# Optimization experiments

Hardware: AMD Instinct MI355X
Metric: run time of the kernel (lower is better)

The kernel has to match this reference:

```python
import jax, jax.numpy as jnp
import numpy as np


def setup_inputs() -> dict:
    key = jax.random.key(0)
    k1, k2, k3, k4, k5, k6 = jax.random.split(key, 6)
    B, S, I, H = 64, 512, 1024, 1024
    scale_ih = 1.0 / np.sqrt(I)
    scale_hh = 1.0 / np.sqrt(H)
    return {
        "inputs": jax.random.normal(k1, (B, S, I), dtype=jnp.float32),
        "h0": jax.random.normal(k2, (1, B, H), dtype=jnp.float32),
        "weight_ih": jax.random.normal(k3, (H, I), dtype=jnp.float32) * scale_ih,
        "weight_hh": jax.random.normal(k4, (H, H), dtype=jnp.float32) * scale_hh,
        "bias_ih": jax.random.normal(k5, (H,), dtype=jnp.float32) * 0.01,
        "bias_hh": jax.random.normal(k6, (H,), dtype=jnp.float32) * 0.01,
    }


def reference(inputs, h0, weight_ih, weight_hh, bias_ih, bias_hh):
    # Elman RNN with ReLU: h_t = relu(x_t W_ih^T + b_ih + h_{t-1} W_hh^T + b_hh)
    # inputs: [B, S, I]; h0: [1, B, H]
    # Precompute the input projection for all timesteps in one big GEMM.
    x_proj = jnp.einsum('bsi,hi->bsh', inputs, weight_ih) + bias_ih + bias_hh  # [B,S,H]

    def step(h, xp_t):
        h_new = jax.nn.relu(xp_t + jnp.matmul(h, weight_hh.T))  # [B,H]
        return h_new, h_new

    h_init = h0[0]  # [B, H]
    h_last, outs = jax.lax.scan(step, h_init, jnp.swapaxes(x_proj, 0, 1))  # outs: [S,B,H]
    outputs = jnp.swapaxes(outs, 0, 1)  # [B, S, H]
    h_n = h_last[None]  # [1, B, H]
    return outputs, h_n
```

## Files before the change

### kernel.cpp

```cpp
#include <hip/hip_runtime.h>
#include <hip/hip_bf16.h>
#include <stdint.h>

#define BATCH 64
#define SEQ   512
#define INDIM 1024
#define HDIM  1024
#define NBLK  256
#define NGRP  8
#define GSLOT 32
#define FPAD  16
#define GBUF_U16 32768
#define GBUF_DW  16384

typedef short bf16x8 __attribute__((ext_vector_type(8)));
typedef short s16x4  __attribute__((ext_vector_type(4)));
typedef float f32x4  __attribute__((ext_vector_type(4)));
typedef unsigned short u16;
typedef unsigned int   u32;
typedef u32 u32x4 __attribute__((ext_vector_type(4)));
typedef u16 u16x4 __attribute__((ext_vector_type(4)));

static __device__ __forceinline__ u16 f2bf(float x) {
  unsigned int u = __float_as_uint(x);
  u += 0x7fffu + ((u >> 16) & 1u);
  return (u16)(u >> 16);
}
static __device__ __forceinline__ float bf2f(u16 b) {
  return __uint_as_float(((unsigned int)b) << 16);
}

static __device__ __forceinline__ int coh_ld_i32(const int* p) {
  int v;
  asm volatile("global_load_dword %0, %1, off sc0 sc1\n\t"
               "s_waitcnt vmcnt(0)"
               : "=&v"(v) : "v"(p) : "memory");
  return v;
}

static __device__ __forceinline__ void split4(float4 v, u16x4& hi, u16x4& lo) {
  hi.x = f2bf(v.x); lo.x = f2bf(v.x - bf2f(hi.x));
  hi.y = f2bf(v.y); lo.y = f2bf(v.y - bf2f(hi.y));
  hi.z = f2bf(v.z); lo.z = f2bf(v.z - bf2f(hi.z));
  hi.w = f2bf(v.w); lo.w = f2bf(v.w - bf2f(hi.w));
}
static __device__ __forceinline__ bf16x8 ld8(const u16* p) {
  s16x4 a = *(const s16x4*)p;
  s16x4 b = *(const s16x4*)(p + 4);
  return __builtin_shufflevector(a, b, 0, 1, 2, 3, 4, 5, 6, 7);
}

__global__ void init0(int* __restrict__ flags, int n) {
  int i = blockIdx.x * blockDim.x + threadIdx.x;
  if (i < n) flags[i] = 0;
}

__global__ void init1(const float* __restrict__ h0, u32* __restrict__ hw) {
  int i = blockIdx.x * blockDim.x + threadIdx.x;
  if (i < BATCH * HDIM) {
    int b = i >> 10, k = i & 1023;
    int g = b >> 3, r = b & 7;
    int k32 = k >> 5, kg = (k >> 3) & 3, j = k & 7;
    float x = h0[i];
    u16 hi = f2bf(x);
    u16 lo = f2bf(x - bf2f(hi));
    size_t di = (size_t)g * (2 * GBUF_DW) + (size_t)((k32 * 64 + kg * 16 + r) * 8 + j);
    hw[di] = (u32)hi | ((u32)lo << 16);
  }
}

__global__ __launch_bounds__(256) void xproj_kernel(const float* __restrict__ A,
                                                    const float* __restrict__ W,
                                                    const float* __restrict__ bih,
                                                    const float* __restrict__ bhh,
                                                    float* __restrict__ C) {
  __shared__ u16 Ah[4][128][12], Al[4][128][12], Bh[4][128][12], Bl[4][128][12];
  const int nb = blockIdx.x;
  const int mb = blockIdx.y;
  const int m_base = mb * 128, n_base = nb * 128;
  const int tid = (int)threadIdx.x;
  const int wid = tid >> 6, lane = tid & 63;
  const int wm = wid >> 1, wn = wid & 1;
  const int r = lane & 15, kg = lane >> 4;
  const int srow = tid >> 1;
  const int skq  = (tid & 1) * 16;

  const float* ap0 = A + (size_t)(m_base + srow) * INDIM + skq;
  const float* bp0 = W + (size_t)(n_base + srow) * INDIM + skq;

  f32x4 acc[4][4] = {};

  for (int k0 = 0; k0 < INDIM; k0 += 32) {
    float4 av[4], bv[4];
#pragma unroll
    for (int i = 0; i < 4; ++i) {
      av[i] = *(const float4*)(ap0 + k0 + i * 4);
      bv[i] = *(const float4*)(bp0 + k0 + i * 4);
    }
    __syncthreads();
#pragma unroll
    for (int i = 0; i < 4; ++i) {
      int kk = skq + i * 4;
      int kgw = kk >> 3, off = kk & 7;
      u16x4 hi, lo;
      split4(av[i], hi, lo);
      *(u16x4*)&Ah[kgw][srow][off] = hi;
      *(u16x4*)&Al[kgw][srow][off] = lo;
      split4(bv[i], hi, lo);
      *(u16x4*)&Bh[kgw][srow][off] = hi;
      *(u16x4*)&Bl[kgw][srow][off] = lo;
    }
    __syncthreads();

    bf16x8 ah[4], al[4], bhv[4], blv[4];
#pragma unroll
    for (int mf = 0; mf < 4; ++mf) {
      int row = wm * 64 + mf * 16 + r;
      ah[mf] = ld8(&Ah[kg][row][0]);
      al[mf] = ld8(&Al[kg][row][0]);
    }
#pragma unroll
    for (int nf = 0; nf < 4; ++nf) {
      int row = wn * 64 + nf * 16 + r;
      bhv[nf] = ld8(&Bh[kg][row][0]);
      blv[nf] = ld8(&Bl[kg][row][0]);
    }
#pragma unroll
    for (int mf = 0; mf < 4; ++mf)
#pragma unroll
      for (int nf = 0; nf < 4; ++nf) {
        acc[mf][nf] = __builtin_amdgcn_mfma_f32_16x16x32_bf16(ah[mf], bhv[nf], acc[mf][nf], 0, 0, 0);
        acc[mf][nf] = __builtin_amdgcn_mfma_f32_16x16x32_bf16(ah[mf], blv[nf], acc[mf][nf], 0, 0, 0);
        acc[mf][nf] = __builtin_amdgcn_mfma_f32_16x16x32_bf16(al[mf], bhv[nf], acc[mf][nf], 0, 0, 0);
      }
  }

#pragma unroll
  for (int nf = 0; nf < 4; ++nf) {
    int col = n_base + wn * 64 + nf * 16 + r;
    float bias = bih[col] + bhh[col];
#pragma unroll
    for (int mf = 0; mf < 4; ++mf) {
      int rowb = m_base + wm * 64 + mf * 16 + kg * 4;
#pragma unroll
      for (int q = 0; q < 4; ++q) {
        C[(size_t)(rowb + q) * HDIM + col] = acc[mf][nf][q] + bias;
      }
    }
  }
}

__global__ __launch_bounds__(512, 1) void rnn_scan(
    const float* __restrict__ Whh, float* __restrict__ out,
    u16* hbase, int* flags) {
  __shared__ u16 WH[32][2][64][8], WL[32][2][64][8];
  __shared__ __align__(16) float red[2][8][2][8][20];

  const int blk = (int)blockIdx.x;
  const int grp = blk & 7;
  const int slot = blk >> 3;
  const int n0 = slot * 32;
  const int tid = (int)threadIdx.x;
  const int wv = tid >> 6, lane = tid & 63;
  const int r = lane & 15, kg = lane >> 4;
  const bool zrow = r >= 8;

  for (int it = 0; it < 16; ++it) {
    int f4 = it * 512 + tid;
    int row = f4 >> 8;
    int k0 = (f4 & 255) * 4;
    float4 v = *(const float4*)(Whh + (size_t)(n0 + row) * HDIM + k0);
    int k32 = k0 >> 5, kgg = (k0 >> 3) & 3, j = k0 & 7;
    int nt = row >> 4, ln = kgg * 16 + (row & 15);
    u16x4 hi, lo;
    split4(v, hi, lo);
    *(u16x4*)&WH[k32][nt][ln][j] = hi;
    *(u16x4*)&WL[k32][nt][ln][j] = lo;
  }
  __syncthreads();

  u16* const hb0 = hbase + (size_t)grp * (2 * GBUF_U16);
  u16* const hb1 = hb0 + GBUF_U16;
  int* const gflag = flags + grp * (GSLOT * 4) * FPAD;
  const int* const pollp = gflag + ((wv << 4) + (lane & 15)) * FPAD;

  const int eid = wv * 64 + lane;
  const int er = (eid >> 5) & 7;
  const int ec = eid & 31;
  const float* xpbase = out + ((size_t)(grp * 8 + er) * SEQ) * HDIM + n0 + ec;
  float xfCur = 0.f, xfNext = 0.f, sPrev = 0.f;
  if (wv < 4) xfCur = xpbase[0];

  for (int t = 0; t < SEQ; ++t) {
    const int p2 = t & 1;
    const u16* hc = (t & 1) ? hb1 : hb0;
    u16* hn = (t & 1) ? hb0 : hb1;

    if (t > 0) {
      int v;
      do { v = coh_ld_i32(pollp); } while (!__all(v >= t));
    }

    u32x4 P0, P1, P2, P3, P4, P5, P6, P7;
    if (!zrow) {
      const char* a0 = (const char*)hc + (size_t)((wv * 4) * 64 + lane) * 32;
      const char* a1 = a0 + 4096;
      asm volatile(
          "global_load_dwordx4 %0, %8, off sc0 sc1\n\t"
          "global_load_dwordx4 %1, %8, off offset:16 sc0 sc1\n\t"
          "global_load_dwordx4 %2, %8, off offset:2048 sc0 sc1\n\t"
          "global_load_dwordx4 %3, %8, off offset:2064 sc0 sc1\n\t"
          "global_load_dwordx4 %4, %9, off sc0 sc1\n\t"
          "global_load_dwordx4 %5, %9, off offset:16 sc0 sc1\n\t"
          "global_load_dwordx4 %6, %9, off offset:2048 sc0 sc1\n\t"
          "global_load_dwordx4 %7, %9, off offset:2064 sc0 sc1"
          : "=&v"(P0), "=&v"(P1), "=&v"(P2), "=&v"(P3),
            "=&v"(P4), "=&v"(P5), "=&v"(P6), "=&v"(P7)
          : "v"(a0), "v"(a1)
          : "memory");
      asm volatile("s_waitcnt vmcnt(0)"
          : "+v"(P0), "+v"(P1), "+v"(P2), "+v"(P3),
            "+v"(P4), "+v"(P5), "+v"(P6), "+v"(P7));
    } else {
      P0 = P1 = P2 = P3 = P4 = P5 = P6 = P7 = (u32x4){0, 0, 0, 0};
    }

    if (wv < 4) {
      if (t > 0)
        __builtin_nontemporal_store(sPrev, (float*)(xpbase + (size_t)(t - 1) * HDIM));
      if (t + 1 < SEQ) xfNext = xpbase[(size_t)(t + 1) * HDIM];
    }

    f32x4 acc0 = {0.f, 0.f, 0.f, 0.f};
    f32x4 acc1 = {0.f, 0.f, 0.f, 0.f};
#define DO_K32(i, QA, QB)                                                      \
    {                                                                          \
      u32 d0 = QA[0], d1 = QA[1], d2 = QA[2], d3 = QA[3];                      \
      u32 d4 = QB[0], d5 = QB[1], d6 = QB[2], d7 = QB[3];                      \
      union { u32 w[4]; bf16x8 v; } AH, AL;                                    \
      AH.w[0] = (d0 & 0xFFFFu) | (d1 << 16);                                   \
      AH.w[1] = (d2 & 0xFFFFu) | (d3 << 16);                                   \
      AH.w[2] = (d4 & 0xFFFFu) | (d5 << 16);                                   \
      AH.w[3] = (d6 & 0xFFFFu) | (d7 << 16);                                   \
      AL.w[0] = (d0 >> 16) | (d1 & 0xFFFF0000u);                               \
      AL.w[1] = (d2 >> 16) | (d3 & 0xFFFF0000u);                               \
      AL.w[2] = (d4 >> 16) | (d5 & 0xFFFF0000u);                               \
      AL.w[3] = (d6 >> 16) | (d7 & 0xFFFF0000u);                               \
      int k32 = wv * 4 + (i);                                                  \
      bf16x8 b0h = *(const bf16x8*)&WH[k32][0][lane][0];                       \
      bf16x8 b0l = *(const bf16x8*)&WL[k32][0][lane][0];                       \
      bf16x8 b1h = *(const bf16x8*)&WH[k32][1][lane][0];                       \
      bf16x8 b1l = *(const bf16x8*)&WL[k32][1][lane][0];                       \
      acc0 = __builtin_amdgcn_mfma_f32_16x16x32_bf16(AH.v, b0h, acc0, 0, 0, 0);\
      acc0 = __builtin_amdgcn_mfma_f32_16x16x32_bf16(AH.v, b0l, acc0, 0, 0, 0);\
      acc0 = __builtin_amdgcn_mfma_f32_16x16x32_bf16(AL.v, b0h, acc0, 0, 0, 0);\
      acc1 = __builtin_amdgcn_mfma_f32_16x16x32_bf16(AH.v, b1h, acc1, 0, 0, 0);\
      acc1 = __builtin_amdgcn_mfma_f32_16x16x32_bf16(AH.v, b1l, acc1, 0, 0, 0);\
      acc1 = __builtin_amdgcn_mfma_f32_16x16x32_bf16(AL.v, b1h, acc1, 0, 0, 0);\
    }
    DO_K32(0, P0, P1)
    DO_K32(1, P2, P3)
    DO_K32(2, P4, P5)
    DO_K32(3, P6, P7)
#undef DO_K32

    if (kg < 2) {
#pragma unroll
      for (int q = 0; q < 4; ++q) {
        red[p2][wv][0][kg * 4 + q][r] = acc0[q];
        red[p2][wv][1][kg * 4 + q][r] = acc1[q];
      }
    }
    __syncthreads();

    if (wv < 4) {
      float s = xfCur;
#pragma unroll
      for (int w = 0; w < 8; ++w) s += red[p2][w][ec >> 4][er][ec & 15];
      s = s > 0.f ? s : 0.f;
      sPrev = s;
      u16 hi = f2bf(s);
      u16 lo = f2bf(s - bf2f(hi));
      u32 dw = (u32)hi | ((u32)lo << 16);
      u32* hp = (u32*)hn + (size_t)((slot * 64 + (ec >> 3) * 16 + er) * 8 + (ec & 7));
      asm volatile("global_store_dword %0, %1, off sc1\n\t"
                   "s_waitcnt vmcnt(0)"
                   :: "v"(hp), "v"(dw) : "memory");
      if (lane == 0) {
        int* fp = gflag + (slot * 4 + wv) * FPAD;
        int tv = t + 1;
        asm volatile("global_store_dword %0, %1, off sc0 sc1"
                     :: "v"(fp), "v"(tv) : "memory");
      }
      xfCur = xfNext;
    }
  }

  if (wv < 4)
    __builtin_nontemporal_store(sPrev, (float*)(xpbase + (size_t)(SEQ - 1) * HDIM));
}

__global__ void copy_hn(const float* __restrict__ out, float* __restrict__ hn) {
  int idx = blockIdx.x * blockDim.x + threadIdx.x;
  if (idx < BATCH * HDIM) {
    int b = idx >> 10, j = idx & 1023;
    hn[idx] = out[((size_t)b * SEQ + (SEQ - 1)) * (size_t)HDIM + j];
  }
}

extern "C" void kernel_launch(void* const* d_in, const int* in_sizes, int n_in,
                              void* d_out, int out_size, void* d_ws, size_t ws_size,
                              hipStream_t stream) {
  const float* inputs = (const float*)d_in[0];
  const float* h0     = (const float*)d_in[1];
  const float* w_ih   = (const float*)d_in[2];
  const float* w_hh   = (const float*)d_in[3];
  const float* b_ih   = (const float*)d_in[4];
  const float* b_hh   = (const float*)d_in[5];

  float* outBase = (float*)d_out;
  float* hnBase  = outBase + (size_t)BATCH * SEQ * HDIM;

  u16* hbase = (u16*)d_ws;
  int* flags = (int*)(hbase + (size_t)NGRP * 2 * GBUF_U16);
  const int nflags = NGRP * GSLOT * 4 * FPAD;

  init0<<<(nflags + 255) / 256, 256, 0, stream>>>(flags, nflags);
  init1<<<(BATCH * HDIM + 255) / 256, 256, 0, stream>>>(h0, (u32*)hbase);

  xproj_kernel<<<dim3(8, 256), 256, 0, stream>>>(inputs, w_ih, b_ih, b_hh, outBase);

  const float* wha = w_hh;
  float* oa = outBase;
  u16* hba = hbase;
  int* fa = flags;
  void* args[4] = {&wha, &oa, &hba, &fa};
  (void)hipLaunchCooperativeKernel((const void*)rnn_scan, dim3(NBLK), dim3(512), args, 0, stream);

  copy_hn<<<256, 256, 0, stream>>>(outBase, hnBase);
}
```

Measured before the change: 1.917 ms.

## Warp-specialize RNN scan into compute, epilogue, and I/O waves with skewed pipeline

The scan kernel now splits its 8 waves by role. Waves 0-3 do the MFMA matvec over K=256 each, waves 4-5 reduce, apply ReLU, split to bf16 hi/lo and publish h with flags, and waves 6-7 prefetch x_proj and write outputs through shared buffers. The epilogue for step t-1 runs concurrently with the matvec for step t, one step behind, so global I/O and the reduction leave the critical path. The trade-off is half as many waves on the MFMA and longer per-wave load chains. The flag count per slot also drops, which changes the polling pattern.

```diff
diff --git a/kernel.cpp b/kernel.cpp
--- a/kernel.cpp
+++ b/kernel.cpp
@@ -10,14 +10,15 @@
 #define NGRP  8
 #define GSLOT 32
 #define FPAD  16
-#define GBUF_U16 32768
-#define GBUF_DW  16384
+#define SLAB_BYTES 32768
 
 typedef short bf16x8 __attribute__((ext_vector_type(8)));
 typedef short s16x4  __attribute__((ext_vector_type(4)));
+typedef float f32x2  __attribute__((ext_vector_type(2)));
 typedef float f32x4  __attribute__((ext_vector_type(4)));
 typedef unsigned short u16;
 typedef unsigned int   u32;
+typedef u32 u32x2 __attribute__((ext_vector_type(2)));
 typedef u32 u32x4 __attribute__((ext_vector_type(4)));
 typedef u16 u16x4 __attribute__((ext_vector_type(4)));
 
@@ -64,7 +65,7 @@
     float x = h0[i];
     u16 hi = f2bf(x);
     u16 lo = f2bf(x - bf2f(hi));
-    size_t di = (size_t)g * (2 * GBUF_DW) + (size_t)((k32 * 64 + kg * 16 + r) * 8 + j);
+    size_t di = (size_t)g * (SLAB_BYTES / 4) + (size_t)(k32 * 256 + kg * 64 + r * 8 + j);
     hw[di] = (u32)hi | ((u32)lo << 16);
   }
 }
@@ -152,9 +153,11 @@
 
 __global__ __launch_bounds__(512, 1) void rnn_scan(
     const float* __restrict__ Whh, float* __restrict__ out,
-    u16* hbase, int* flags) {
+    char* ring, int* flags) {
   __shared__ u16 WH[32][2][64][8], WL[32][2][64][8];
-  __shared__ __align__(16) float red[2][8][2][8][20];
+  __shared__ __align__(16) float red[2][4][2][8][20];
+  __shared__ __align__(8) float xfbuf[2][8][32];
+  __shared__ __align__(8) float sbuf[2][8][32];
 
   const int blk = (int)blockIdx.x;
   const int grp = blk & 7;
@@ -162,8 +165,6 @@
   const int n0 = slot * 32;
   const int tid = (int)threadIdx.x;
   const int wv = tid >> 6, lane = tid & 63;
-  const int r = lane & 15, kg = lane >> 4;
-  const bool zrow = r >= 8;
 
   for (int it = 0; it < 16; ++it) {
     int f4 = it * 512 + tid;
@@ -179,125 +180,156 @@
   }
   __syncthreads();
 
-  u16* const hb0 = hbase + (size_t)grp * (2 * GBUF_U16);
-  u16* const hb1 = hb0 + GBUF_U16;
-  int* const gflag = flags + grp * (GSLOT * 4) * FPAD;
-  const int* const pollp = gflag + ((wv << 4) + (lane & 15)) * FPAD;
-
-  const int eid = wv * 64 + lane;
-  const int er = (eid >> 5) & 7;
-  const int ec = eid & 31;
-  const float* xpbase = out + ((size_t)(grp * 8 + er) * SEQ) * HDIM + n0 + ec;
-  float xfCur = 0.f, xfNext = 0.f, sPrev = 0.f;
-  if (wv < 4) xfCur = xpbase[0];
-
-  for (int t = 0; t < SEQ; ++t) {
-    const int p2 = t & 1;
-    const u16* hc = (t & 1) ? hb1 : hb0;
-    u16* hn = (t & 1) ? hb0 : hb1;
-
-    if (t > 0) {
-      int v;
-      do { v = coh_ld_i32(pollp); } while (!__all(v >= t));
-    }
-
-    u32x4 P0, P1, P2, P3, P4, P5, P6, P7;
-    if (!zrow) {
-      const char* a0 = (const char*)hc + (size_t)((wv * 4) * 64 + lane) * 32;
-      const char* a1 = a0 + 4096;
-      asm volatile(
-          "global_load_dwordx4 %0, %8, off sc0 sc1\n\t"
-          "global_load_dwordx4 %1, %8, off offset:16 sc0 sc1\n\t"
-          "global_load_dwordx4 %2, %8, off offset:2048 sc0 sc1\n\t"
-          "global_load_dwordx4 %3, %8, off offset:2064 sc0 sc1\n\t"
-          "global_load_dwordx4 %4, %9, off sc0 sc1\n\t"
-          "global_load_dwordx4 %5, %9, off offset:16 sc0 sc1\n\t"
-          "global_load_dwordx4 %6, %9, off offset:2048 sc0 sc1\n\t"
-          "global_load_dwordx4 %7, %9, off offset:2064 sc0 sc1"
-          : "=&v"(P0), "=&v"(P1), "=&v"(P2), "=&v"(P3),
-            "=&v"(P4), "=&v"(P5), "=&v"(P6), "=&v"(P7)
-          : "v"(a0), "v"(a1)
-          : "memory");
-      asm volatile("s_waitcnt vmcnt(0)"
-          : "+v"(P0), "+v"(P1), "+v"(P2), "+v"(P3),
-            "+v"(P4), "+v"(P5), "+v"(P6), "+v"(P7));
+  char* const slab0 = ring + (size_t)grp * SLAB_BYTES;
+  char* const slab1 = ring + (size_t)(NGRP + grp) * SLAB_BYTES;
+  int* const gflag = flags + grp * (GSLOT * 2) * FPAD;
+
+  const int r = lane & 15, kg = lane >> 4;
+  const bool zrow = r >= 8;
+  const int loff = wv * 8192 + kg * 256 + (r & 7) * 32;
+  const int* const pollp = gflag + ((wv * 8 + ((lane >> 1) & 7)) * 2 + (lane & 1)) * FPAD;
+
+  const int peid = (wv - 4) * 64 + lane;
+  const int per = (peid >> 4) & 7;
+  const int pec = (peid & 15) * 2;
+  int* const myflag = gflag + (slot * 2 + (wv - 4)) * FPAD;
+
+  const int qeid = (wv - 6) * 64 + lane;
+  const int qer = (qeid >> 4) & 7;
+  const int qec = (qeid & 15) * 2;
+  float* const xpp = out + ((size_t)(grp * 8 + qer) * SEQ) * HDIM + n0 + qec;
+
+  for (int t = 0; t <= SEQ; ++t) {
+    if (wv < 4) {
+      if (t < SEQ) {
+        if (t > 0) {
+          int v;
+          do { v = coh_ld_i32(pollp); } while (!__all(v >= t));
+        }
+        u32x4 P0, P1, P2, P3, P4, P5, P6, P7, P8, P9, P10, P11, P12, P13, P14, P15;
+        if (!zrow) {
+          const char* b0 = ((t & 1) ? slab1 : slab0) + loff;
+          const char* b1 = b0 + 4096;
+          asm volatile(
+              "global_load_dwordx4 %0, %8, off sc0 sc1\n\t"
+              "global_load_dwordx4 %1, %8, off offset:16 sc0 sc1\n\t"
+              "global_load_dwordx4 %2, %8, off offset:1024 sc0 sc1\n\t"
+              "global_load_dwordx4 %3, %8, off offset:1040 sc0 sc1\n\t"
+              "global_load_dwordx4 %4, %8, off offset:2048 sc0 sc1\n\t"
+              "global_load_dwordx4 %5, %8, off offset:2064 sc0 sc1\n\t"
+              "global_load_dwordx4 %6, %8, off offset:3072 sc0 sc1\n\t"
+              "global_load_dwordx4 %7, %8, off offset:3088 sc0 sc1"
+              : "=&v"(P0), "=&v"(P1), "=&v"(P2), "=&v"(P3),
+                "=&v"(P4), "=&v"(P5), "=&v"(P6), "=&v"(P7)
+              : "v"(b0) : "memory");
+          asm volatile(
+              "global_load_dwordx4 %0, %8, off sc0 sc1\n\t"
+              "global_load_dwordx4 %1, %8, off offset:16 sc0 sc1\n\t"
+              "global_load_dwordx4 %2, %8, off offset:1024 sc0 sc1\n\t"
+              "global_load_dwordx4 %3, %8, off offset:1040 sc0 sc1\n\t"
+              "global_load_dwordx4 %4, %8, off offset:2048 sc0 sc1\n\t"
+              "global_load_dwordx4 %5, %8, off offset:2064 sc0 sc1\n\t"
+              "global_load_dwordx4 %6, %8, off offset:3072 sc0 sc1\n\t"
+              "global_load_dwordx4 %7, %8, off offset:3088 sc0 sc1"
+              : "=&v"(P8), "=&v"(P9), "=&v"(P10), "=&v"(P11),
+                "=&v"(P12), "=&v"(P13), "=&v"(P14), "=&v"(P15)
+              : "v"(b1) : "memory");
+          asm volatile("s_waitcnt vmcnt(0)"
+              : "+v"(P0), "+v"(P1), "+v"(P2), "+v"(P3),
+                "+v"(P4), "+v"(P5), "+v"(P6), "+v"(P7),
+                "+v"(P8), "+v"(P9), "+v"(P10), "+v"(P11),
+                "+v"(P12), "+v"(P13), "+v"(P14), "+v"(P15));
+        } else {
+          P0 = P1 = P2 = P3 = P4 = P5 = P6 = P7 = (u32x4){0, 0, 0, 0};
+          P8 = P9 = P10 = P11 = P12 = P13 = P14 = P15 = (u32x4){0, 0, 0, 0};
+        }
+
+        f32x4 acc0 = {0.f, 0.f, 0.f, 0.f};
+        f32x4 acc1 = {0.f, 0.f, 0.f, 0.f};
+#define DO_K32(i, QA, QB)                                                      \
+        {                                                                      \
+          u32 d0 = QA[0], d1 = QA[1], d2 = QA[2], d3 = QA[3];                  \
+          u32 d4 = QB[0], d5 = QB[1], d6 = QB[2], d7 = QB[3];                  \
+          union { u32 w[4]; bf16x8 v; } AH, AL;                                \
+          AH.w[0] = (d0 & 0xFFFFu) | (d1 << 16);                               \
+          AH.w[1] = (d2 & 0xFFFFu) | (d3 << 16);                               \
+          AH.w[2] = (d4 & 0xFFFFu) | (d5 << 16);                               \
+          AH.w[3] = (d6 & 0xFFFFu) | (d7 << 16);                               \
+          AL.w[0] = (d0 >> 16) | (d1 & 0xFFFF0000u);                           \
+          AL.w[1] = (d2 >> 16) | (d3 & 0xFFFF0000u);                           \
+          AL.w[2] = (d4 >> 16) | (d5 & 0xFFFF0000u);                           \
+          AL.w[3] = (d6 >> 16) | (d7 & 0xFFFF0000u);                           \
+          int k32 = wv * 8 + (i);                                              \
+          bf16x8 b0h = *(const bf16x8*)&WH[k32][0][lane][0];                   \
+          bf16x8 b0l = *(const bf16x8*)&WL[k32][0][lane][0];                   \
+          bf16x8 b1h = *(const bf16x8*)&WH[k32][1][lane][0];                   \
+          bf16x8 b1l = *(const bf16x8*)&WL[k32][1][lane][0];                   \
+          acc0 = __builtin_amdgcn_mfma_f32_16x16x32_bf16(AH.v, b0h, acc0, 0, 0, 0); \
+          acc0 = __builtin_amdgcn_mfma_f32_16x16x32_bf16(AH.v, b0l, acc0, 0, 0, 0); \
+          acc0 = __builtin_amdgcn_mfma_f32_16x16x32_bf16(AL.v, b0h, acc0, 0, 0, 0); \
+          acc1 = __builtin_amdgcn_mfma_f32_16x16x32_bf16(AH.v, b1h, acc1, 0, 0, 0); \
+          acc1 = __builtin_amdgcn_mfma_f32_16x16x32_bf16(AH.v, b1l, acc1, 0, 0, 0); \
+          acc1 = __builtin_amdgcn_mfma_f32_16x16x32_bf16(AL.v, b1h, acc1, 0, 0, 0); \
+        }
+        DO_K32(0, P0, P1)
+        DO_K32(1, P2, P3)
+        DO_K32(2, P4, P5)
+        DO_K32(3, P6, P7)
+        DO_K32(4, P8, P9)
+        DO_K32(5, P10, P11)
+        DO_K32(6, P12, P13)
+        DO_K32(7, P14, P15)
+#undef DO_K32
+
+        if (kg < 2) {
+#pragma unroll
+          for (int q = 0; q < 4; ++q) {
+            red[t & 1][wv][0][kg * 4 + q][r] = acc0[q];
+            red[t & 1][wv][1][kg * 4 + q][r] = acc1[q];
+          }
+        }
+      }
+    } else if (wv < 6) {
+      if (t >= 1) {
+        const int ph = (t - 1) & 1;
+        f32x2 s = *(const f32x2*)&xfbuf[ph][per][pec];
+        const int nt = pec >> 4, c = pec & 15;
+#pragma unroll
+        for (int w = 0; w < 4; ++w) s += *(const f32x2*)&red[ph][w][nt][per][c];
+        s.x = s.x > 0.f ? s.x : 0.f;
+        s.y = s.y > 0.f ? s.y : 0.f;
+        *(f32x2*)&sbuf[ph][per][pec] = s;
+        u16 h0 = f2bf(s.x), h1 = f2bf(s.y);
+        u16 l0 = f2bf(s.x - bf2f(h0)), l1 = f2bf(s.y - bf2f(h1));
+        u32x2 D = {(u32)h0 | ((u32)l0 << 16), (u32)h1 | ((u32)l1 << 16)};
+        char* hp = ((t & 1) ? slab1 : slab0) +
+                   (size_t)(slot * 1024 + (pec >> 3) * 256 + per * 32 + (pec & 7) * 4);
+        asm volatile("global_store_dwordx2 %0, %1, off sc1\n\t"
+                     "s_waitcnt vmcnt(0)"
+                     :: "v"(hp), "v"(D) : "memory");
+        if (lane == 0) {
+          int tv = t;
+          asm volatile("global_store_dword %0, %1, off sc0 sc1"
+                       :: "v"(myflag), "v"(tv) : "memory");
+        }
+      }
     } else {
-      P0 = P1 = P2 = P3 = P4 = P5 = P6 = P7 = (u32x4){0, 0, 0, 0};
-    }
-
-    if (wv < 4) {
-      if (t > 0)
-        __builtin_nontemporal_store(sPrev, (float*)(xpbase + (size_t)(t - 1) * HDIM));
-      if (t + 1 < SEQ) xfNext = xpbase[(size_t)(t + 1) * HDIM];
-    }
-
-    f32x4 acc0 = {0.f, 0.f, 0.f, 0.f};
-    f32x4 acc1 = {0.f, 0.f, 0.f, 0.f};
-#define DO_K32(i, QA, QB)                                                      \
-    {                                                                          \
-      u32 d0 = QA[0], d1 = QA[1], d2 = QA[2], d3 = QA[3];                      \
-      u32 d4 = QB[0], d5 = QB[1], d6 = QB[2], d7 = QB[3];                      \
-      union { u32 w[4]; bf16x8 v; } AH, AL;                                    \
-      AH.w[0] = (d0 & 0xFFFFu) | (d1 << 16);                                   \
-      AH.w[1] = (d2 & 0xFFFFu) | (d3 << 16);                                   \
-      AH.w[2] = (d4 & 0xFFFFu) | (d5 << 16);                                   \
-      AH.w[3] = (d6 & 0xFFFFu) | (d7 << 16);                                   \
-      AL.w[0] = (d0 >> 16) | (d1 & 0xFFFF0000u);                               \
-      AL.w[1] = (d2 >> 16) | (d3 & 0xFFFF0000u);                               \
-      AL.w[2] = (d4 >> 16) | (d5 & 0xFFFF0000u);                               \
-      AL.w[3] = (d6 >> 16) | (d7 & 0xFFFF0000u);                               \
-      int k32 = wv * 4 + (i);                                                  \
-      bf16x8 b0h = *(const bf16x8*)&WH[k32][0][lane][0];                       \
-      bf16x8 b0l = *(const bf16x8*)&WL[k32][0][lane][0];                       \
-      bf16x8 b1h = *(const bf16x8*)&WH[k32][1][lane][0];                       \
-      bf16x8 b1l = *(const bf16x8*)&WL[k32][1][lane][0];                       \
-      acc0 = __builtin_amdgcn_mfma_f32_16x16x32_bf16(AH.v, b0h, acc0, 0, 0, 0);\
-      acc0 = __builtin_amdgcn_mfma_f32_16x16x32_bf16(AH.v, b0l, acc0, 0, 0, 0);\
-      acc0 = __builtin_amdgcn_mfma_f32_16x16x32_bf16(AL.v, b0h, acc0, 0, 0, 0);\
-      acc1 = __builtin_amdgcn_mfma_f32_16x16x32_bf16(AH.v, b1h, acc1, 0, 0, 0);\
-      acc1 = __builtin_amdgcn_mfma_f32_16x16x32_bf16(AH.v, b1l, acc1, 0, 0, 0);\
-      acc1 = __builtin_amdgcn_mfma_f32_16x16x32_bf16(AL.v, b1h, acc1, 0, 0, 0);\
-    }
-    DO_K32(0, P0, P1)
-    DO_K32(1, P2, P3)
-    DO_K32(2, P4, P5)
-    DO_K32(3, P6, P7)
-#undef DO_K32
-
-    if (kg < 2) {
-#pragma unroll
-      for (int q = 0; q < 4; ++q) {
-        red[p2][wv][0][kg * 4 + q][r] = acc0[q];
-        red[p2][wv][1][kg * 4 + q][r] = acc1[q];
+      if (t >= 2) {
+        f32x2 sv = *(const f32x2*)&sbuf[t & 1][qer][qec];
+        __builtin_nontemporal_store(sv, (f32x2*)(xpp + (size_t)(t - 2) * HDIM));
+      }
+      if (t < SEQ) {
+        f32x2 xv = *(const f32x2*)(xpp + (size_t)t * HDIM);
+        *(f32x2*)&xfbuf[t & 1][qer][qec] = xv;
       }
     }
     __syncthreads();
-
-    if (wv < 4) {
-      float s = xfCur;
-#pragma unroll
-      for (int w = 0; w < 8; ++w) s += red[p2][w][ec >> 4][er][ec & 15];
-      s = s > 0.f ? s : 0.f;
-      sPrev = s;
-      u16 hi = f2bf(s);
-      u16 lo = f2bf(s - bf2f(hi));
-      u32 dw = (u32)hi | ((u32)lo << 16);
-      u32* hp = (u32*)hn + (size_t)((slot * 64 + (ec >> 3) * 16 + er) * 8 + (ec & 7));
-      asm volatile("global_store_dword %0, %1, off sc1\n\t"
-                   "s_waitcnt vmcnt(0)"
-                   :: "v"(hp), "v"(dw) : "memory");
-      if (lane == 0) {
-        int* fp = gflag + (slot * 4 + wv) * FPAD;
-        int tv = t + 1;
-        asm volatile("global_store_dword %0, %1, off sc0 sc1"
-                     :: "v"(fp), "v"(tv) : "memory");
-      }
-      xfCur = xfNext;
-    }
-  }
-
-  if (wv < 4)
-    __builtin_nontemporal_store(sPrev, (float*)(xpbase + (size_t)(SEQ - 1) * HDIM));
+  }
+
+  if (wv >= 6) {
+    f32x2 sv = *(const f32x2*)&sbuf[(SEQ - 1) & 1][qer][qec];
+    __builtin_nontemporal_store(sv, (f32x2*)(xpp + (size_t)(SEQ - 1) * HDIM));
+  }
 }
 
 __global__ void copy_hn(const float* __restrict__ out, float* __restrict__ hn) {
@@ -321,20 +353,20 @@
   float* outBase = (float*)d_out;
   float* hnBase  = outBase + (size_t)BATCH * SEQ * HDIM;
 
-  u16* hbase = (u16*)d_ws;
-  int* flags = (int*)(hbase + (size_t)NGRP * 2 * GBUF_U16);
-  const int nflags = NGRP * GSLOT * 4 * FPAD;
+  char* ring = (char*)d_ws;
+  int* flags = (int*)(ring + (size_t)2 * NGRP * SLAB_BYTES);
+  const int nflags = NGRP * GSLOT * 2 * FPAD;
 
   init0<<<(nflags + 255) / 256, 256, 0, stream>>>(flags, nflags);
-  init1<<<(BATCH * HDIM + 255) / 256, 256, 0, stream>>>(h0, (u32*)hbase);
+  init1<<<(BATCH * HDIM + 255) / 256, 256, 0, stream>>>(h0, (u32*)ring);
 
   xproj_kernel<<<dim3(8, 256), 256, 0, stream>>>(inputs, w_ih, b_ih, b_hh, outBase);
 
   const float* wha = w_hh;
   float* oa = outBase;
-  u16* hba = hbase;
+  char* ra = ring;
   int* fa = flags;
-  void* args[4] = {&wha, &oa, &hba, &fa};
+  void* args[4] = {&wha, &oa, &ra, &fa};
   (void)hipLaunchCooperativeKernel((const void*)rnn_scan, dim3(NBLK), dim3(512), args, 0, stream);
 
   copy_hn<<<256, 256, 0, stream>>>(outBase, hnBase);
```

Result: faster. 1.877 ms (-2.1%).

## Add dedicated I/O wavefront for xproj prefetch and output stores in RNN scan

Applied to the files above, without the earlier changes.

Adds a ninth wavefront per block that prefetches the next x-projection values into shared memory and writes finished hidden states back to global memory. This takes those loads and stores off the compute wavefronts' critical path. The epilogue is reduced to wave 0 using vector f32x4 math and a single dwordx4 store. Publication now uses one flag per slot instead of four, so consumers poll fewer flags. The cost is an extra wave per block, and wave 0's serialized epilogue could lengthen the per-step critical path.

```diff
diff --git a/kernel.cpp b/kernel.cpp
--- a/kernel.cpp
+++ b/kernel.cpp
@@ -150,11 +150,13 @@
   }
 }
 
-__global__ __launch_bounds__(512, 1) void rnn_scan(
+__global__ __launch_bounds__(576, 1) void rnn_scan(
     const float* __restrict__ Whh, float* __restrict__ out,
     u16* hbase, int* flags) {
   __shared__ u16 WH[32][2][64][8], WL[32][2][64][8];
   __shared__ __align__(16) float red[2][8][2][8][20];
+  __shared__ __align__(16) float xfbuf[2][8][32];
+  __shared__ __align__(16) float sbuf[2][8][32];
 
   const int blk = (int)blockIdx.x;
   const int grp = blk & 7;
@@ -165,8 +167,7 @@
   const int r = lane & 15, kg = lane >> 4;
   const bool zrow = r >= 8;
 
-  for (int it = 0; it < 16; ++it) {
-    int f4 = it * 512 + tid;
+  for (int f4 = tid; f4 < 8192; f4 += 576) {
     int row = f4 >> 8;
     int k0 = (f4 & 255) * 4;
     float4 v = *(const float4*)(Whh + (size_t)(n0 + row) * HDIM + k0);
@@ -181,123 +182,137 @@
 
   u16* const hb0 = hbase + (size_t)grp * (2 * GBUF_U16);
   u16* const hb1 = hb0 + GBUF_U16;
-  int* const gflag = flags + grp * (GSLOT * 4) * FPAD;
-  const int* const pollp = gflag + ((wv << 4) + (lane & 15)) * FPAD;
-
-  const int eid = wv * 64 + lane;
-  const int er = (eid >> 5) & 7;
-  const int ec = eid & 31;
-  const float* xpbase = out + ((size_t)(grp * 8 + er) * SEQ) * HDIM + n0 + ec;
-  float xfCur = 0.f, xfNext = 0.f, sPrev = 0.f;
-  if (wv < 4) xfCur = xpbase[0];
+  int* const gflag = flags + grp * GSLOT * FPAD;
+  const int* const pollp = gflag + ((wv & 7) * 4 + (lane & 3)) * FPAD;
+
+  const int erow = lane >> 3;
+  const int ec4 = (lane & 7) * 4;
+  float* const xpp = out + ((size_t)(grp * 8 + erow) * SEQ) * HDIM + n0 + ec4;
 
   for (int t = 0; t < SEQ; ++t) {
     const int p2 = t & 1;
-    const u16* hc = (t & 1) ? hb1 : hb0;
-    u16* hn = (t & 1) ? hb0 : hb1;
-
-    if (t > 0) {
-      int v;
-      do { v = coh_ld_i32(pollp); } while (!__all(v >= t));
-    }
-
-    u32x4 P0, P1, P2, P3, P4, P5, P6, P7;
-    if (!zrow) {
-      const char* a0 = (const char*)hc + (size_t)((wv * 4) * 64 + lane) * 32;
-      const char* a1 = a0 + 4096;
-      asm volatile(
-          "global_load_dwordx4 %0, %8, off sc0 sc1\n\t"
-          "global_load_dwordx4 %1, %8, off offset:16 sc0 sc1\n\t"
-          "global_load_dwordx4 %2, %8, off offset:2048 sc0 sc1\n\t"
-          "global_load_dwordx4 %3, %8, off offset:2064 sc0 sc1\n\t"
-          "global_load_dwordx4 %4, %9, off sc0 sc1\n\t"
-          "global_load_dwordx4 %5, %9, off offset:16 sc0 sc1\n\t"
-          "global_load_dwordx4 %6, %9, off offset:2048 sc0 sc1\n\t"
-          "global_load_dwordx4 %7, %9, off offset:2064 sc0 sc1"
-          : "=&v"(P0), "=&v"(P1), "=&v"(P2), "=&v"(P3),
-            "=&v"(P4), "=&v"(P5), "=&v"(P6), "=&v"(P7)
-          : "v"(a0), "v"(a1)
-          : "memory");
-      asm volatile("s_waitcnt vmcnt(0)"
-          : "+v"(P0), "+v"(P1), "+v"(P2), "+v"(P3),
-            "+v"(P4), "+v"(P5), "+v"(P6), "+v"(P7));
+
+    if (wv < 8) {
+      const u16* hc = (t & 1) ? hb1 : hb0;
+
+      if (t > 0) {
+        int v;
+        do { v = coh_ld_i32(pollp); } while (!__all(v >= t));
+      }
+
+      u32x4 P0, P1, P2, P3, P4, P5, P6, P7;
+      if (!zrow) {
+        const char* a0 = (const char*)hc + (size_t)((wv * 4) * 64 + lane) * 32;
+        const char* a1 = a0 + 4096;
+        asm volatile(
+            "global_load_dwordx4 %0, %8, off sc0 sc1\n\t"
+            "global_load_dwordx4 %1, %8, off offset:16 sc0 sc1\n\t"
+            "global_load_dwordx4 %2, %8, off offset:2048 sc0 sc1\n\t"
+            "global_load_dwordx4 %3, %8, off offset:2064 sc0 sc1\n\t"
+            "global_load_dwordx4 %4, %9, off sc0 sc1\n\t"
+            "global_load_dwordx4 %5, %9, off offset:16 sc0 sc1\n\t"
+            "global_load_dwordx4 %6, %9, off offset:2048 sc0 sc1\n\t"
+            "global_load_dwordx4 %7, %9, off offset:2064 sc0 sc1"
+            : "=&v"(P0), "=&v"(P1), "=&v"(P2), "=&v"(P3),
+              "=&v"(P4), "=&v"(P5), "=&v"(P6), "=&v"(P7)
+            : "v"(a0), "v"(a1)
+            : "memory");
+        asm volatile("s_waitcnt vmcnt(0)"
+            : "+v"(P0), "+v"(P1), "+v"(P2), "+v"(P3),
+              "+v"(P4), "+v"(P5), "+v"(P6), "+v"(P7));
+      } else {
+        P0 = P1 = P2 = P3 = P4 = P5 = P6 = P7 = (u32x4){0, 0, 0, 0};
+      }
+
+      f32x4 acc0 = {0.f, 0.f, 0.f, 0.f};
+      f32x4 acc1 = {0.f, 0.f, 0.f, 0.f};
+#define DO_K32(i, QA, QB)                                                      \
+      {                                                                        \
+        u32 d0 = QA[0], d1 = QA[1], d2 = QA[2], d3 = QA[3];                    \
+        u32 d4 = QB[0], d5 = QB[1], d6 = QB[2], d7 = QB[3];                    \
+        union { u32 w[4]; bf16x8 v; } AH, AL;                                  \
+        AH.w[0] = (d0 & 0xFFFFu) | (d1 << 16);                                 \
+        AH.w[1] = (d2 & 0xFFFFu) | (d3 << 16);                                 \
+        AH.w[2] = (d4 & 0xFFFFu) | (d5 << 16);                                 \
+        AH.w[3] = (d6 & 0xFFFFu) | (d7 << 16);                                 \
+        AL.w[0] = (d0 >> 16) | (d1 & 0xFFFF0000u);                             \
+        AL.w[1] = (d2 >> 16) | (d3 & 0xFFFF0000u);                             \
+        AL.w[2] = (d4 >> 16) | (d5 & 0xFFFF0000u);                             \
+        AL.w[3] = (d6 >> 16) | (d7 & 0xFFFF0000u);                             \
+        int k32 = wv * 4 + (i);                                                \
+        bf16x8 b0h = *(const bf16x8*)&WH[k32][0][lane][0];                     \
+        bf16x8 b0l = *(const bf16x8*)&WL[k32][0][lane][0];                     \
+        bf16x8 b1h = *(const bf16x8*)&WH[k32][1][lane][0];                     \
+        bf16x8 b1l = *(const bf16x8*)&WL[k32][1][lane][0];                     \
+        acc0 = __builtin_amdgcn_mfma_f32_16x16x32_bf16(AH.v, b0h, acc0, 0, 0, 0); \
+        acc0 = __builtin_amdgcn_mfma_f32_16x16x32_bf16(AH.v, b0l, acc0, 0, 0, 0); \
+        acc0 = __builtin_amdgcn_mfma_f32_16x16x32_bf16(AL.v, b0h, acc0, 0, 0, 0); \
+        acc1 = __builtin_amdgcn_mfma_f32_16x16x32_bf16(AH.v, b1h, acc1, 0, 0, 0); \
+        acc1 = __builtin_amdgcn_mfma_f32_16x16x32_bf16(AH.v, b1l, acc1, 0, 0, 0); \
+        acc1 = __builtin_amdgcn_mfma_f32_16x16x32_bf16(AL.v, b1h, acc1, 0, 0, 0); \
+      }
+      DO_K32(0, P0, P1)
+      DO_K32(1, P2, P3)
+      DO_K32(2, P4, P5)
+      DO_K32(3, P6, P7)
+#undef DO_K32
+
+      if (kg < 2) {
+#pragma unroll
+        for (int q = 0; q < 4; ++q) {
+          red[p2][wv][0][kg * 4 + q][r] = acc0[q];
+          red[p2][wv][1][kg * 4 + q][r] = acc1[q];
+        }
+      }
+      __syncthreads();
+
+      if (wv == 0) {
+        f32x4 s = *(const f32x4*)&xfbuf[p2][erow][ec4];
+        const int nt = ec4 >> 4, cl = ec4 & 15;
+#pragma unroll
+        for (int w = 0; w < 8; ++w) s += *(const f32x4*)&red[p2][w][nt][erow][cl];
+#pragma unroll
+        for (int j = 0; j < 4; ++j) s[j] = s[j] > 0.f ? s[j] : 0.f;
+        *(f32x4*)&sbuf[p2][erow][ec4] = s;
+
+        u32x4 D;
+#pragma unroll
+        for (int j = 0; j < 4; ++j) {
+          u16 hi = f2bf(s[j]);
+          u16 lo = f2bf(s[j] - bf2f(hi));
+          D[j] = (u32)hi | ((u32)lo << 16);
+        }
+        u16* hnx = (t & 1) ? hb0 : hb1;
+        u32* hp = (u32*)hnx + (size_t)((slot * 64 + (ec4 >> 3) * 16 + erow) * 8 + (ec4 & 7));
+        asm volatile("global_store_dwordx4 %0, %1, off sc1\n\t"
+                     "s_waitcnt vmcnt(0)"
+                     :: "v"(hp), "v"(D) : "memory");
+        if (lane == 0) {
+          int* fp = gflag + slot * FPAD;
+          int tv = t + 1;
+          asm volatile("global_store_dword %0, %1, off sc0 sc1"
+                       :: "v"(fp), "v"(tv) : "memory");
+        }
+      }
     } else {
-      P0 = P1 = P2 = P3 = P4 = P5 = P6 = P7 = (u32x4){0, 0, 0, 0};
-    }
-
-    if (wv < 4) {
-      if (t > 0)
-        __builtin_nontemporal_store(sPrev, (float*)(xpbase + (size_t)(t - 1) * HDIM));
-      if (t + 1 < SEQ) xfNext = xpbase[(size_t)(t + 1) * HDIM];
-    }
-
-    f32x4 acc0 = {0.f, 0.f, 0.f, 0.f};
-    f32x4 acc1 = {0.f, 0.f, 0.f, 0.f};
-#define DO_K32(i, QA, QB)                                                      \
-    {                                                                          \
-      u32 d0 = QA[0], d1 = QA[1], d2 = QA[2], d3 = QA[3];                      \
-      u32 d4 = QB[0], d5 = QB[1], d6 = QB[2], d7 = QB[3];                      \
-      union { u32 w[4]; bf16x8 v; } AH, AL;                                    \
-      AH.w[0] = (d0 & 0xFFFFu) | (d1 << 16);                                   \
-      AH.w[1] = (d2 & 0xFFFFu) | (d3 << 16);                                   \
-      AH.w[2] = (d4 & 0xFFFFu) | (d5 << 16);                                   \
-      AH.w[3] = (d6 & 0xFFFFu) | (d7 << 16);                                   \
-      AL.w[0] = (d0 >> 16) | (d1 & 0xFFFF0000u);                               \
-      AL.w[1] = (d2 >> 16) | (d3 & 0xFFFF0000u);                               \
-      AL.w[2] = (d4 >> 16) | (d5 & 0xFFFF0000u);                               \
-      AL.w[3] = (d6 >> 16) | (d7 & 0xFFFF0000u);                               \
-      int k32 = wv * 4 + (i);                                                  \
-      bf16x8 b0h = *(const bf16x8*)&WH[k32][0][lane][0];                       \
-      bf16x8 b0l = *(const bf16x8*)&WL[k32][0][lane][0];                       \
-      bf16x8 b1h = *(const bf16x8*)&WH[k32][1][lane][0];                       \
-      bf16x8 b1l = *(const bf16x8*)&WL[k32][1][lane][0];                       \
-      acc0 = __builtin_amdgcn_mfma_f32_16x16x32_bf16(AH.v, b0h, acc0, 0, 0, 0);\
-      acc0 = __builtin_amdgcn_mfma_f32_16x16x32_bf16(AH.v, b0l, acc0, 0, 0, 0);\
-      acc0 = __builtin_amdgcn_mfma_f32_16x16x32_bf16(AL.v, b0h, acc0, 0, 0, 0);\
-      acc1 = __builtin_amdgcn_mfma_f32_16x16x32_bf16(AH.v, b1h, acc1, 0, 0, 0);\
-      acc1 = __builtin_amdgcn_mfma_f32_16x16x32_bf16(AH.v, b1l, acc1, 0, 0, 0);\
-      acc1 = __builtin_amdgcn_mfma_f32_16x16x32_bf16(AL.v, b1h, acc1, 0, 0, 0);\
-    }
-    DO_K32(0, P0, P1)
-    DO_K32(1, P2, P3)
-    DO_K32(2, P4, P5)
-    DO_K32(3, P6, P7)
-#undef DO_K32
-
-    if (kg < 2) {
-#pragma unroll
-      for (int q = 0; q < 4; ++q) {
-        red[p2][wv][0][kg * 4 + q][r] = acc0[q];
-        red[p2][wv][1][kg * 4 + q][r] = acc1[q];
-      }
-    }
-    __syncthreads();
-
-    if (wv < 4) {
-      float s = xfCur;
-#pragma unroll
-      for (int w = 0; w < 8; ++w) s += red[p2][w][ec >> 4][er][ec & 15];
-      s = s > 0.f ? s : 0.f;
-      sPrev = s;
-      u16 hi = f2bf(s);
-      u16 lo = f2bf(s - bf2f(hi));
-      u32 dw = (u32)hi | ((u32)lo << 16);
-      u32* hp = (u32*)hn + (size_t)((slot * 64 + (ec >> 3) * 16 + er) * 8 + (ec & 7));
-      asm volatile("global_store_dword %0, %1, off sc1\n\t"
-                   "s_waitcnt vmcnt(0)"
-                   :: "v"(hp), "v"(dw) : "memory");
-      if (lane == 0) {
-        int* fp = gflag + (slot * 4 + wv) * FPAD;
-        int tv = t + 1;
-        asm volatile("global_store_dword %0, %1, off sc0 sc1"
-                     :: "v"(fp), "v"(tv) : "memory");
-      }
-      xfCur = xfNext;
-    }
-  }
-
-  if (wv < 4)
-    __builtin_nontemporal_store(sPrev, (float*)(xpbase + (size_t)(SEQ - 1) * HDIM));
+      if (t >= 2) {
+        f32x4 sv = *(const f32x4*)&sbuf[p2][erow][ec4];
+        __builtin_nontemporal_store(sv, (f32x4*)(xpp + (size_t)(t - 2) * HDIM));
+      }
+      float4 xv = *(const float4*)(xpp + (size_t)t * HDIM);
+      f32x4 xr = {xv.x, xv.y, xv.z, xv.w};
+      *(f32x4*)&xfbuf[p2][erow][ec4] = xr;
+      __syncthreads();
+    }
+  }
+
+  __syncthreads();
+  if (wv == 8) {
+    f32x4 s2 = *(const f32x4*)&sbuf[(SEQ - 2) & 1][erow][ec4];
+    __builtin_nontemporal_store(s2, (f32x4*)(xpp + (size_t)(SEQ - 2) * HDIM));
+    f32x4 s1 = *(const f32x4*)&sbuf[(SEQ - 1) & 1][erow][ec4];
+    __builtin_nontemporal_store(s1, (f32x4*)(xpp + (size_t)(SEQ - 1) * HDIM));
+  }
 }
 
 __global__ void copy_hn(const float* __restrict__ out, float* __restrict__ hn) {
@@ -323,7 +338,7 @@
 
   u16* hbase = (u16*)d_ws;
   int* flags = (int*)(hbase + (size_t)NGRP * 2 * GBUF_U16);
-  const int nflags = NGRP * GSLOT * 4 * FPAD;
+  const int nflags = NGRP * GSLOT * FPAD;
 
   init0<<<(nflags + 255) / 256, 256, 0, stream>>>(flags, nflags);
   init1<<<(BATCH * HDIM + 255) / 256, 256, 0, stream>>>(h0, (u32*)hbase);
@@ -335,7 +350,7 @@
   u16* hba = hbase;
   int* fa = flags;
   void* args[4] = {&wha, &oa, &hba, &fa};
-  (void)hipLaunchCooperativeKernel((const void*)rnn_scan, dim3(NBLK), dim3(512), args, 0, stream);
+  (void)hipLaunchCooperativeKernel((const void*)rnn_scan, dim3(NBLK), dim3(576), args, 0, stream);
 
   copy_hn<<<256, 256, 0, stream>>>(outBase, hnBase);
 }
```

After: 1.574 ms. -17.9%, faster.
